# Kernel tuning notes

Hardware: AMD Instinct MI355X
Metric: run time of the kernel (lower is better)

The kernel has to match this reference:

```python
import jax, jax.numpy as jnp
import numpy as np

S, B, L, D, H, NOP = 4, 8, 512, 128, 128, 64  # segments, batch, seg_len, input_dim, hidden, n_operators
W = S * L  # 2048 total words
FT = 0.1   # forget-gate floor


def _norm_mat(m):
    # divide each row by its count of nonzero entries (torch normalize_matrix)
    cnt = (m != 0).sum(-1, keepdims=True).astype(m.dtype)
    return m / (cnt + 1e-30)


def _l2(x):
    return x / (jnp.linalg.norm(x, axis=-1, keepdims=True) + 1e-30)


def setup_inputs() -> dict:
    key = jax.random.key(0)
    ks = jax.random.split(key, 16)
    word_outputs = jax.random.normal(ks[0], (S, B, L, D), jnp.float32)
    node_hidden = jax.random.normal(ks[1], (B, D), jnp.float32)
    op_embedding = jax.random.normal(ks[2], (B, NOP, D), jnp.float32)
    word_operator = (jax.random.uniform(ks[3], (B, W, NOP)) < 0.05).astype(jnp.float32)
    word_word = (jax.random.uniform(ks[4], (B, W, W)) < 0.02).astype(jnp.float32)
    depend_relation = (jax.random.uniform(ks[5], (S, B, L, L)) < 0.05).astype(jnp.float32)
    word_exist_matrix = (jax.random.uniform(ks[6], (B, W, W)) < 0.9).astype(jnp.float32)
    word_exist_sequence = (jax.random.uniform(ks[7], (B, W)) < 0.9).astype(jnp.float32)
    goal_word = (jax.random.uniform(ks[8], (B, W)) < 0.2).astype(jnp.float32)

    def lin(k, fi, fo):
        k1, k2 = jax.random.split(k)
        s = 1.0 / np.sqrt(fi).astype(np.float32)
        return (jax.random.uniform(k1, (fi, fo), jnp.float32, -s, s),
                jax.random.uniform(k2, (fo,), jnp.float32, -s, s))

    o_w_W, o_w_b = lin(ks[9], D, H)
    wk_W, wk_b = lin(ks[10], D, H)
    ws_W, ws_b = lin(ks[11], D, H)
    up_W, up_b = lin(ks[12], 3 * H, D)
    wg_W, wg_b = lin(ks[13], D, D)
    fg_W, fg_b = lin(ks[14], 2 * D, D)
    return dict(word_outputs=word_outputs, node_hidden=node_hidden, op_embedding=op_embedding,
                word_operator=word_operator, word_word=word_word, depend_relation=depend_relation,
                word_exist_matrix=word_exist_matrix, word_exist_sequence=word_exist_sequence,
                goal_word=goal_word, o_w_W=o_w_W, o_w_b=o_w_b, wk_W=wk_W, wk_b=wk_b,
                ws_W=ws_W, ws_b=ws_b, up_W=up_W, up_b=up_b, wg_W=wg_W, wg_b=wg_b,
                fg_W=fg_W, fg_b=fg_b)


def reference(word_outputs, node_hidden, op_embedding, word_operator, word_word,
              depend_relation, word_exist_matrix, word_exist_sequence, goal_word,
              o_w_W, o_w_b, wk_W, wk_b, ws_W, ws_b, up_W, up_b, wg_W, wg_b, fg_W, fg_b):
    # cat(word_outputs, dim=1) -> [B, W, D]
    all_word = word_outputs.transpose(1, 0, 2, 3).reshape(B, W, D)
    # operator aggregation: [B,W,NOP] @ o_w(op_embedding) -> [B,W,H], L2-normalized
    word_o = _l2(jnp.einsum('bwo,boh->bwh', word_operator, op_embedding @ o_w_W + o_w_b))
    # knowledge aggregation over masked word-word adjacency
    adj_k = _norm_mat(word_word * word_exist_matrix)
    word_w_k = _l2(jnp.einsum('bvw,bwh->bvh', adj_k, all_word @ wk_W + wk_b))
    # per-segment dependency aggregation, then concat along word dim
    seg = jnp.einsum('sbij,sbjh->sbih', _norm_mat(depend_relation), word_outputs @ ws_W + ws_b)
    word_w_s = _l2(seg.transpose(1, 0, 2, 3).reshape(B, W, H))
    neighbor = jnp.concatenate([word_o, word_w_k, word_w_s], axis=-1)  # [B, W, 3H]
    word_updated = jax.nn.relu(neighbor @ up_W + up_b)  # [B, W, D]
    # goal pooling: bmm([B,1,W],[B,W,D]) -> [B,D]
    gw = _norm_mat(goal_word * word_exist_sequence)
    goal_w = jnp.einsum('bw,bwd->bd', gw, word_updated)
    goal_updated = jax.nn.relu(goal_w @ wg_W + wg_b)
    forget = jax.nn.sigmoid(jnp.concatenate([goal_w, node_hidden], axis=-1) @ fg_W + fg_b)
    return jnp.maximum(forget, FT) * node_hidden + (1.0 - forget) * goal_updated
```

## Files before the change

### kernel.cpp

```cpp
#include <hip/hip_runtime.h>
#include <math.h>

#define Sn 4
#define Bn 8
#define Ln 512
#define Dn 128
#define Hn 128
#define NOPn 64
#define Wn 2048


__device__ __forceinline__ float bf2f(unsigned short u) {
    return __uint_as_float(((unsigned int)u) << 16);
}
__device__ __forceinline__ float bflo(unsigned int u) {
    return __uint_as_float(u << 16);
}
__device__ __forceinline__ float bfhi(unsigned int u) {
    return __uint_as_float(u & 0xFFFF0000u);
}
__device__ __forceinline__ unsigned short f2bf(float f) {
    unsigned int u = __float_as_uint(f);
    return (unsigned short)((u + 0x7FFFu + ((u >> 16) & 1u)) >> 16);
}

typedef __attribute__((ext_vector_type(8))) short bf16x8;
typedef __attribute__((ext_vector_type(4))) float f32x4;

__global__ __launch_bounds__(256) void prep_k(const float* __restrict__ A,
                                              const float* __restrict__ W1,
                                              const float* __restrict__ W2,
                                              const float* __restrict__ b1,
                                              const float* __restrict__ b2,
                                              unsigned short* __restrict__ C1,
                                              unsigned short* __restrict__ C2,
                                              const float* __restrict__ ope,
                                              const float* __restrict__ owW,
                                              const float* __restrict__ owb,
                                              unsigned short* __restrict__ oph,
                                              const float* __restrict__ goal,
                                              const float* __restrict__ wes,
                                              int* __restrict__ widx,
                                              int* __restrict__ wcnt,
                                              float* __restrict__ gwacc,
                                              const float* __restrict__ upW,
                                              unsigned short* __restrict__ upWbf) {
    __shared__ __align__(16) unsigned char smem[33792];
    const int bid = blockIdx.x, tid = threadIdx.x;

    if (bid < 256) {
        unsigned short (*WT)[132] = reinterpret_cast<unsigned short(*)[132]>(smem);
        const int m0 = bid * 64;
        const int lane = tid & 63, wr = tid >> 6;
        const int rloc = lane & 15, bsel = lane >> 4;

        bf16x8 af[4];
        const float* Arow = A + (size_t)(m0 + wr * 16 + rloc) * 128;
#pragma unroll
        for (int ks = 0; ks < 4; ++ks) {
            float4 a0 = *reinterpret_cast<const float4*>(Arow + ks * 32 + 4 * bsel);
            float4 a1 = *reinterpret_cast<const float4*>(Arow + ks * 32 + 16 + 4 * bsel);
            af[ks][0] = (short)f2bf(a0.x); af[ks][1] = (short)f2bf(a0.y);
            af[ks][2] = (short)f2bf(a0.z); af[ks][3] = (short)f2bf(a0.w);
            af[ks][4] = (short)f2bf(a1.x); af[ks][5] = (short)f2bf(a1.y);
            af[ks][6] = (short)f2bf(a1.z); af[ks][7] = (short)f2bf(a1.w);
        }

#pragma unroll
        for (int mat = 0; mat < 2; ++mat) {
            const float* Wsrc = mat ? W2 : W1;
            const float* bias = mat ? b2 : b1;
            unsigned short* Cdst = mat ? C2 : C1;
            __syncthreads();
            for (int idx = tid; idx < 128 * 128; idx += 256) {
                const int k = idx >> 7, c = idx & 127;
                WT[c][k] = f2bf(Wsrc[k * 128 + c]);
            }
            __syncthreads();

            f32x4 acc[8];
#pragma unroll
            for (int tl = 0; tl < 8; ++tl) acc[tl] = (f32x4){0.f, 0.f, 0.f, 0.f};
#pragma unroll
            for (int ks = 0; ks < 4; ++ks) {
#pragma unroll
                for (int tl = 0; tl < 8; ++tl) {
                    const unsigned short* p = &WT[tl * 16 + rloc][ks * 32 + 4 * bsel];
                    bf16x8 bfv;
#pragma unroll
                    for (int j = 0; j < 4; ++j) {
                        bfv[j]     = (short)p[j];
                        bfv[4 + j] = (short)p[16 + j];
                    }
                    acc[tl] = __builtin_amdgcn_mfma_f32_16x16x32_bf16(
                        af[ks], bfv, acc[tl], 0, 0, 0);
                }
            }
#pragma unroll
            for (int tl = 0; tl < 8; ++tl) {
                const int col = tl * 16 + rloc;
                const float bv = bias[col];
#pragma unroll
                for (int q = 0; q < 4; ++q) {
                    const int row = m0 + wr * 16 + bsel * 4 + q;
                    Cdst[(size_t)row * 128 + col] = f2bf(acc[tl][q] + bv);
                }
            }
        }
    } else if (bid < 264) {
        float (*lA)[68]   = reinterpret_cast<float(*)[68]>(smem);
        float (*lW1)[132] = reinterpret_cast<float(*)[132]>(smem + 8704);
        const int m0 = (bid - 256) * 64;
        float acc[4][8] = {};
        const int r0 = (tid & 15) * 4;
        const int h0 = (tid >> 4) * 8;
        for (int k0 = 0; k0 < 128; k0 += 32) {
            __syncthreads();
            {
                const int r = tid >> 2, kk = (tid & 3) * 8;
                const float* src = ope + (size_t)(m0 + r) * 128 + (k0 + kk);
                float4 v0 = reinterpret_cast<const float4*>(src)[0];
                float4 v1 = reinterpret_cast<const float4*>(src)[1];
                lA[kk + 0][r] = v0.x; lA[kk + 1][r] = v0.y;
                lA[kk + 2][r] = v0.z; lA[kk + 3][r] = v0.w;
                lA[kk + 4][r] = v1.x; lA[kk + 5][r] = v1.y;
                lA[kk + 6][r] = v1.z; lA[kk + 7][r] = v1.w;
            }
            {
                const int kk = tid >> 3, hh = (tid & 7) * 16;
                const float* src = owW + (size_t)(k0 + kk) * 128 + hh;
#pragma unroll
                for (int q = 0; q < 4; ++q) {
                    float4 v = reinterpret_cast<const float4*>(src)[q];
                    lW1[kk][hh + 4 * q + 0] = v.x; lW1[kk][hh + 4 * q + 1] = v.y;
                    lW1[kk][hh + 4 * q + 2] = v.z; lW1[kk][hh + 4 * q + 3] = v.w;
                }
            }
            __syncthreads();
#pragma unroll
            for (int k = 0; k < 32; ++k) {
                float4 a  = *reinterpret_cast<const float4*>(&lA[k][r0]);
                float4 w0 = *reinterpret_cast<const float4*>(&lW1[k][h0]);
                float4 w1 = *reinterpret_cast<const float4*>(&lW1[k][h0 + 4]);
                float av[4] = {a.x, a.y, a.z, a.w};
                float wv[8] = {w0.x, w0.y, w0.z, w0.w, w1.x, w1.y, w1.z, w1.w};
#pragma unroll
                for (int i = 0; i < 4; ++i)
#pragma unroll
                    for (int j = 0; j < 8; ++j) acc[i][j] = fmaf(av[i], wv[j], acc[i][j]);
            }
        }
#pragma unroll
        for (int i = 0; i < 4; ++i) {
            alignas(16) unsigned short us[8];
#pragma unroll
            for (int j = 0; j < 8; ++j) us[j] = f2bf(acc[i][j] + owb[h0 + j]);
            *reinterpret_cast<uint4*>(oph + (size_t)(m0 + r0 + i) * 128 + h0) =
                *reinterpret_cast<const uint4*>(us);
        }
    } else if (bid < 272) {
        int* cnt = reinterpret_cast<int*>(smem);
        const int b = bid - 264;
        if (tid == 0) *cnt = 0;
        __syncthreads();
#pragma unroll
        for (int j = 0; j < 8; ++j) {
            const int w = tid * 8 + j;
            if (goal[b * Wn + w] != 0.f && wes[b * Wn + w] != 0.f) {
                const int p = atomicAdd(cnt, 1);
                if (p < 512) widx[b * 512 + p] = w;
            }
        }
        __syncthreads();
        if (tid == 0) wcnt[b] = *cnt < 512 ? *cnt : 512;
    } else if (bid == 272) {
        for (int idx = tid; idx < 1024; idx += 256) gwacc[idx] = 0.f;
    } else {
        const int base = (bid - 273) * 24576;
        for (int e = base + tid * 4; e < base + 24576; e += 1024) {
            float4 v = *reinterpret_cast<const float4*>(upW + e);
            alignas(8) unsigned short u[4] = {f2bf(v.x), f2bf(v.y), f2bf(v.z), f2bf(v.w)};
            *reinterpret_cast<uint2*>(upWbf + e) = *reinterpret_cast<const uint2*>(u);
        }
    }
}

__global__ __launch_bounds__(256) void mega_agg7(const int* __restrict__ widx,
                                                 const int* __restrict__ wcnt,
                                                 const float* __restrict__ ww,
                                                 const float* __restrict__ wem,
                                                 const float* __restrict__ dep,
                                                 const float* __restrict__ wop,
                                                 const unsigned short* __restrict__ oph,
                                                 const unsigned short* __restrict__ wkh,
                                                 const unsigned short* __restrict__ wsh,
                                                 const unsigned short* __restrict__ upWbf,
                                                 const float* __restrict__ upb,
                                                 float* __restrict__ gwacc) {
    const int bid = blockIdx.x;
    const int b = bid & 7, i = bid >> 3;
    if (i >= wcnt[b]) return;
    const int w_dst = widx[b * 512 + i];
    const int t = threadIdx.x;
    const int lane = t & 63, wv = t >> 6;

    __shared__ int kidx[512];
    __shared__ int sidx[256];
    __shared__ int kn, sn;
    __shared__ float part1[4][128];
    __shared__ float part2[4][128];
    __shared__ float nbL[384];
    __shared__ float gp16[16][128];
    if (t == 0) { kn = 0; sn = 0; }
    __syncthreads();

    const float* wwr = ww  + ((size_t)(b * Wn + w_dst)) * Wn;
    const float* wmr = wem + ((size_t)(b * Wn + w_dst)) * Wn;
#pragma unroll
    for (int q = 0; q < 2; ++q) {
        const int e0 = q * 1024 + t * 4;
        float4 v = *reinterpret_cast<const float4*>(wwr + e0);
        float4 m = *reinterpret_cast<const float4*>(wmr + e0);
        float vv[4] = {v.x, v.y, v.z, v.w};
        float mm[4] = {m.x, m.y, m.z, m.w};
#pragma unroll
        for (int j = 0; j < 4; ++j)
            if (vv[j] != 0.f && mm[j] != 0.f) {
                int p = atomicAdd(&kn, 1);
                if (p < 512) kidx[p] = e0 + j;
            }
    }
    const int sD = w_dst >> 9, lD = w_dst & 511;
    if (t < 128) {
        const float* dr = dep + ((size_t)((sD * Bn + b) * Ln + lD)) * Ln + t * 4;
        float4 v = *reinterpret_cast<const float4*>(dr);
        float vv[4] = {v.x, v.y, v.z, v.w};
#pragma unroll
        for (int j = 0; j < 4; ++j)
            if (vv[j] != 0.f) {
                int p = atomicAdd(&sn, 1);
                if (p < 256) sidx[p] = t * 4 + j;
            }
    }
    float m_op = 0.f;
    if (wv == 3) m_op = wop[((size_t)(b * Wn + w_dst)) * NOPn + lane];
    __syncthreads();

    const int nk = kn < 512 ? kn : 512;
    const int ns = sn < 256 ? sn : 256;

    {
        const int hl = lane >> 5, c = lane & 31;
        float a0 = 0.f, a1 = 0.f, a2 = 0.f, a3 = 0.f;
        for (int p = wv * 2 + hl; p < nk; p += 8) {
            const int w = kidx[p];
            const int s = w >> 9, l = w & 511;
            ushort4 x = *reinterpret_cast<const ushort4*>(
                wkh + ((size_t)((s * Bn + b) * Ln + l)) * Hn + c * 4);
            a0 += bf2f(x.x); a1 += bf2f(x.y); a2 += bf2f(x.z); a3 += bf2f(x.w);
        }
        a0 += __shfl_xor(a0, 32); a1 += __shfl_xor(a1, 32);
        a2 += __shfl_xor(a2, 32); a3 += __shfl_xor(a3, 32);
        if (hl == 0) {
            part1[wv][c * 4 + 0] = a0; part1[wv][c * 4 + 1] = a1;
            part1[wv][c * 4 + 2] = a2; part1[wv][c * 4 + 3] = a3;
        }
    }
    {
        const int hl = lane >> 5, c = lane & 31;
        const unsigned short* base = wsh + (size_t)((sD * Bn + b) * Ln) * Hn + c * 4;
        float a0 = 0.f, a1 = 0.f, a2 = 0.f, a3 = 0.f;
        for (int p = wv * 2 + hl; p < ns; p += 8) {
            ushort4 x = *reinterpret_cast<const ushort4*>(base + (size_t)sidx[p] * Hn);
            a0 += bf2f(x.x); a1 += bf2f(x.y); a2 += bf2f(x.z); a3 += bf2f(x.w);
        }
        a0 += __shfl_xor(a0, 32); a1 += __shfl_xor(a1, 32);
        a2 += __shfl_xor(a2, 32); a3 += __shfl_xor(a3, 32);
        if (hl == 0) {
            part2[wv][c * 4 + 0] = a0; part2[wv][c * 4 + 1] = a1;
            part2[wv][c * 4 + 2] = a2; part2[wv][c * 4 + 3] = a3;
        }
    }
    if (wv == 3) {
        unsigned long long bal = __ballot(m_op != 0.f);
        float a0 = 0.f, a1 = 0.f;
        const unsigned short* base = oph + (size_t)b * NOPn * Hn + 2 * lane;
        while (bal) {
            const int o = __ffsll(bal) - 1;
            bal &= bal - 1;
            ushort2 v = *reinterpret_cast<const ushort2*>(base + o * Hn);
            a0 += bf2f(v.x);
            a1 += bf2f(v.y);
        }
        float ss = a0 * a0 + a1 * a1;
#pragma unroll
        for (int off = 1; off < 64; off <<= 1) ss += __shfl_xor(ss, off);
        const float sc = 1.f / (sqrtf(ss) + 1e-30f);
        nbL[2 * lane]     = a0 * sc;
        nbL[2 * lane + 1] = a1 * sc;
    }
    __syncthreads();

    if (wv == 0) {
        float s0 = 0.f, s1 = 0.f;
#pragma unroll
        for (int q = 0; q < 4; ++q) {
            s0 += part1[q][2 * lane];
            s1 += part1[q][2 * lane + 1];
        }
        float ss = s0 * s0 + s1 * s1;
#pragma unroll
        for (int off = 1; off < 64; off <<= 1) ss += __shfl_xor(ss, off);
        const float sc = 1.f / (sqrtf(ss) + 1e-30f);
        nbL[128 + 2 * lane]     = s0 * sc;
        nbL[128 + 2 * lane + 1] = s1 * sc;
    } else if (wv == 1) {
        float s0 = 0.f, s1 = 0.f;
#pragma unroll
        for (int q = 0; q < 4; ++q) {
            s0 += part2[q][2 * lane];
            s1 += part2[q][2 * lane + 1];
        }
        float ss = s0 * s0 + s1 * s1;
#pragma unroll
        for (int off = 1; off < 64; off <<= 1) ss += __shfl_xor(ss, off);
        const float sc = 1.f / (sqrtf(ss) + 1e-30f);
        nbL[256 + 2 * lane]     = s0 * sc;
        nbL[256 + 2 * lane + 1] = s1 * sc;
    }
    __syncthreads();

    {
        const int i8 = (t & 15) * 8, j = t >> 4;
        float a[8] = {};
#pragma unroll
        for (int r = 0; r < 24; ++r) {
            const int k = r * 16 + j;
            const uint4 w = *reinterpret_cast<const uint4*>(upWbf + (size_t)k * 128 + i8);
            const float x = nbL[k];
            a[0] = fmaf(x, bflo(w.x), a[0]); a[1] = fmaf(x, bfhi(w.x), a[1]);
            a[2] = fmaf(x, bflo(w.y), a[2]); a[3] = fmaf(x, bfhi(w.y), a[3]);
            a[4] = fmaf(x, bflo(w.z), a[4]); a[5] = fmaf(x, bfhi(w.z), a[5]);
            a[6] = fmaf(x, bflo(w.w), a[6]); a[7] = fmaf(x, bfhi(w.w), a[7]);
        }
#pragma unroll
        for (int q = 0; q < 8; ++q) gp16[j][i8 + q] = a[q];
    }
    __syncthreads();
    if (t < 128) {
        float g = upb[t];
#pragma unroll
        for (int j = 0; j < 16; ++j) g += gp16[j][t];
        g = fmaxf(g, 0.f);
        atomicAdd(&gwacc[b * 128 + t], g);
    }
}

__global__ __launch_bounds__(128) void final4_k(const int* __restrict__ wcnt,
                                                const float* __restrict__ gwacc,
                                                const float* __restrict__ nh,
                                                const float* __restrict__ wgW,
                                                const float* __restrict__ wgb,
                                                const float* __restrict__ fgW,
                                                const float* __restrict__ fgb,
                                                float* __restrict__ out) {
    const int b = blockIdx.x, t = threadIdx.x;
    __shared__ float gw[Dn], nhs[Dn];
    const float inv = 1.f / ((float)wcnt[b] + 1e-30f);
    gw[t]  = gwacc[b * Dn + t] * inv;
    nhs[t] = nh[b * Dn + t];
    __syncthreads();
    float gu = wgb[t];
    for (int d = 0; d < Dn; ++d) gu = fmaf(gw[d], wgW[d * Dn + t], gu);
    gu = fmaxf(gu, 0.f);
    float fg = fgb[t];
    for (int d = 0; d < Dn; ++d) fg = fmaf(gw[d], fgW[d * Dn + t], fg);
    for (int d = 0; d < Dn; ++d) fg = fmaf(nhs[d], fgW[(Dn + d) * Dn + t], fg);
    const float forget = 1.f / (1.f + expf(-fg));
    out[b * Dn + t] = fmaxf(forget, 0.1f) * nhs[t] + (1.f - forget) * gu;
}

extern "C" void kernel_launch(void* const* d_in, const int* in_sizes, int n_in,
                              void* d_out, int out_size, void* d_ws, size_t ws_size,
                              hipStream_t stream) {
    (void)in_sizes; (void)n_in; (void)out_size; (void)ws_size;
    const float* word_outputs        = (const float*)d_in[0];
    const float* node_hidden         = (const float*)d_in[1];
    const float* op_embedding        = (const float*)d_in[2];
    const float* word_operator       = (const float*)d_in[3];
    const float* word_word           = (const float*)d_in[4];
    const float* depend_relation     = (const float*)d_in[5];
    const float* word_exist_matrix   = (const float*)d_in[6];
    const float* word_exist_sequence = (const float*)d_in[7];
    const float* goal_word           = (const float*)d_in[8];
    const float* o_w_W = (const float*)d_in[9];
    const float* o_w_b = (const float*)d_in[10];
    const float* wk_W  = (const float*)d_in[11];
    const float* wk_b  = (const float*)d_in[12];
    const float* ws_W  = (const float*)d_in[13];
    const float* ws_b  = (const float*)d_in[14];
    const float* up_W  = (const float*)d_in[15];
    const float* up_b  = (const float*)d_in[16];
    const float* wg_W  = (const float*)d_in[17];
    const float* wg_b  = (const float*)d_in[18];
    const float* fg_W  = (const float*)d_in[19];
    const float* fg_b  = (const float*)d_in[20];
    float* out = (float*)d_out;

    char* ws = (char*)d_ws;
    unsigned short* oph   = (unsigned short*)(ws + 0);
    unsigned short* wkh   = (unsigned short*)(ws + (1u << 20));
    unsigned short* wsh   = (unsigned short*)(ws + (5u << 20));
    int* widx             = (int*)(ws + (9u << 20));
    int* wcnt             = (int*)(ws + (9u << 20) + 32768);
    float* gwacc          = (float*)(ws + (9u << 20) + 65536);
    unsigned short* upWbf = (unsigned short*)(ws + (9u << 20) + 131072);

    prep_k<<<275, 256, 0, stream>>>(word_outputs, wk_W, ws_W, wk_b, ws_b, wkh, wsh,
                                    op_embedding, o_w_W, o_w_b, oph,
                                    goal_word, word_exist_sequence, widx, wcnt, gwacc,
                                    up_W, upWbf);
    mega_agg7<<<4096, 256, 0, stream>>>(widx, wcnt, word_word, word_exist_matrix,
                                        depend_relation, word_operator, oph, wkh, wsh,
                                        upWbf, up_b, gwacc);
    final4_k<<<8, 128, 0, stream>>>(wcnt, gwacc, node_hidden,
                                    wg_W, wg_b, fg_W, fg_b, out);
}
```

Baseline: 334.9 us.

## Replace shared-memory atomic index compaction with per-wave ballot gather; MFMA for op projection

The aggregation kernel no longer builds index lists in shared memory with atomics followed by a block barrier. Each wave scans its own slice of the word-word, mask and dependency rows, ballots the nonzero positions, and gathers the matching hidden rows directly, two rows per iteration split across the half-waves. This removes the atomic contention, the index buffers and one __syncthreads, at the cost of more divergent ballot loops. Separately, the operator-embedding projection blocks in the prep kernel now reuse the bf16 MFMA path instead of a scalar FP32 GEMM, which lowers that projection's precision to bf16 inputs.

Measured after the change: 343.7 us. +2.6%, slower.

```diff
diff --git a/kernel.cpp b/kernel.cpp
--- a/kernel.cpp
+++ b/kernel.cpp
@@ -48,14 +48,16 @@
     __shared__ __align__(16) unsigned char smem[33792];
     const int bid = blockIdx.x, tid = threadIdx.x;
 
-    if (bid < 256) {
+    if (bid < 264) {
         unsigned short (*WT)[132] = reinterpret_cast<unsigned short(*)[132]>(smem);
-        const int m0 = bid * 64;
+        const bool dual = bid < 256;
+        const int m0 = dual ? bid * 64 : (bid - 256) * 64;
+        const float* Asrc = dual ? A : ope;
         const int lane = tid & 63, wr = tid >> 6;
         const int rloc = lane & 15, bsel = lane >> 4;
 
         bf16x8 af[4];
-        const float* Arow = A + (size_t)(m0 + wr * 16 + rloc) * 128;
+        const float* Arow = Asrc + (size_t)(m0 + wr * 16 + rloc) * 128;
 #pragma unroll
         for (int ks = 0; ks < 4; ++ks) {
             float4 a0 = *reinterpret_cast<const float4*>(Arow + ks * 32 + 4 * bsel);
@@ -66,11 +68,11 @@
             af[ks][6] = (short)f2bf(a1.z); af[ks][7] = (short)f2bf(a1.w);
         }
 
-#pragma unroll
-        for (int mat = 0; mat < 2; ++mat) {
-            const float* Wsrc = mat ? W2 : W1;
-            const float* bias = mat ? b2 : b1;
-            unsigned short* Cdst = mat ? C2 : C1;
+        const int nmat = dual ? 2 : 1;
+        for (int mat = 0; mat < nmat; ++mat) {
+            const float* Wsrc = dual ? (mat ? W2 : W1) : owW;
+            const float* bias = dual ? (mat ? b2 : b1) : owb;
+            unsigned short* Cdst = dual ? (mat ? C2 : C1) : oph;
             __syncthreads();
             for (int idx = tid; idx < 128 * 128; idx += 256) {
                 const int k = idx >> 7, c = idx & 127;
@@ -106,57 +108,6 @@
                     Cdst[(size_t)row * 128 + col] = f2bf(acc[tl][q] + bv);
                 }
             }
-        }
-    } else if (bid < 264) {
-        float (*lA)[68]   = reinterpret_cast<float(*)[68]>(smem);
-        float (*lW1)[132] = reinterpret_cast<float(*)[132]>(smem + 8704);
-        const int m0 = (bid - 256) * 64;
-        float acc[4][8] = {};
-        const int r0 = (tid & 15) * 4;
-        const int h0 = (tid >> 4) * 8;
-        for (int k0 = 0; k0 < 128; k0 += 32) {
-            __syncthreads();
-            {
-                const int r = tid >> 2, kk = (tid & 3) * 8;
-                const float* src = ope + (size_t)(m0 + r) * 128 + (k0 + kk);
-                float4 v0 = reinterpret_cast<const float4*>(src)[0];
-                float4 v1 = reinterpret_cast<const float4*>(src)[1];
-                lA[kk + 0][r] = v0.x; lA[kk + 1][r] = v0.y;
-                lA[kk + 2][r] = v0.z; lA[kk + 3][r] = v0.w;
-                lA[kk + 4][r] = v1.x; lA[kk + 5][r] = v1.y;
-                lA[kk + 6][r] = v1.z; lA[kk + 7][r] = v1.w;
-            }
-            {
-                const int kk = tid >> 3, hh = (tid & 7) * 16;
-                const float* src = owW + (size_t)(k0 + kk) * 128 + hh;
-#pragma unroll
-                for (int q = 0; q < 4; ++q) {
-                    float4 v = reinterpret_cast<const float4*>(src)[q];
-                    lW1[kk][hh + 4 * q + 0] = v.x; lW1[kk][hh + 4 * q + 1] = v.y;
-                    lW1[kk][hh + 4 * q + 2] = v.z; lW1[kk][hh + 4 * q + 3] = v.w;
-                }
-            }
-            __syncthreads();
-#pragma unroll
-            for (int k = 0; k < 32; ++k) {
-                float4 a  = *reinterpret_cast<const float4*>(&lA[k][r0]);
-                float4 w0 = *reinterpret_cast<const float4*>(&lW1[k][h0]);
-                float4 w1 = *reinterpret_cast<const float4*>(&lW1[k][h0 + 4]);
-                float av[4] = {a.x, a.y, a.z, a.w};
-                float wv[8] = {w0.x, w0.y, w0.z, w0.w, w1.x, w1.y, w1.z, w1.w};
-#pragma unroll
-                for (int i = 0; i < 4; ++i)
-#pragma unroll
-                    for (int j = 0; j < 8; ++j) acc[i][j] = fmaf(av[i], wv[j], acc[i][j]);
-            }
-        }
-#pragma unroll
-        for (int i = 0; i < 4; ++i) {
-            alignas(16) unsigned short us[8];
-#pragma unroll
-            for (int j = 0; j < 8; ++j) us[j] = f2bf(acc[i][j] + owb[h0 + j]);
-            *reinterpret_cast<uint4*>(oph + (size_t)(m0 + r0 + i) * 128 + h0) =
-                *reinterpret_cast<const uint4*>(us);
         }
     } else if (bid < 272) {
         int* cnt = reinterpret_cast<int*>(smem);
@@ -185,79 +136,64 @@
     }
 }
 
-__global__ __launch_bounds__(256) void mega_agg7(const int* __restrict__ widx,
-                                                 const int* __restrict__ wcnt,
-                                                 const float* __restrict__ ww,
-                                                 const float* __restrict__ wem,
-                                                 const float* __restrict__ dep,
-                                                 const float* __restrict__ wop,
-                                                 const unsigned short* __restrict__ oph,
-                                                 const unsigned short* __restrict__ wkh,
-                                                 const unsigned short* __restrict__ wsh,
-                                                 const unsigned short* __restrict__ upWbf,
-                                                 const float* __restrict__ upb,
-                                                 float* __restrict__ gwacc) {
+__global__ __launch_bounds__(256) void mega_agg10(const int* __restrict__ widx,
+                                                  const int* __restrict__ wcnt,
+                                                  const float* __restrict__ ww,
+                                                  const float* __restrict__ wem,
+                                                  const float* __restrict__ dep,
+                                                  const float* __restrict__ wop,
+                                                  const unsigned short* __restrict__ oph,
+                                                  const unsigned short* __restrict__ wkh,
+                                                  const unsigned short* __restrict__ wsh,
+                                                  const unsigned short* __restrict__ upWbf,
+                                                  const float* __restrict__ upb,
+                                                  float* __restrict__ gwacc) {
     const int bid = blockIdx.x;
     const int b = bid & 7, i = bid >> 3;
     if (i >= wcnt[b]) return;
     const int w_dst = widx[b * 512 + i];
     const int t = threadIdx.x;
     const int lane = t & 63, wv = t >> 6;
-
-    __shared__ int kidx[512];
-    __shared__ int sidx[256];
-    __shared__ int kn, sn;
+    const int hl = lane >> 5, c = lane & 31;
+
     __shared__ float part1[4][128];
     __shared__ float part2[4][128];
     __shared__ float nbL[384];
     __shared__ float gp16[16][128];
-    if (t == 0) { kn = 0; sn = 0; }
-    __syncthreads();
-
-    const float* wwr = ww  + ((size_t)(b * Wn + w_dst)) * Wn;
-    const float* wmr = wem + ((size_t)(b * Wn + w_dst)) * Wn;
-#pragma unroll
-    for (int q = 0; q < 2; ++q) {
-        const int e0 = q * 1024 + t * 4;
-        float4 v = *reinterpret_cast<const float4*>(wwr + e0);
-        float4 m = *reinterpret_cast<const float4*>(wmr + e0);
-        float vv[4] = {v.x, v.y, v.z, v.w};
-        float mm[4] = {m.x, m.y, m.z, m.w};
-#pragma unroll
-        for (int j = 0; j < 4; ++j)
-            if (vv[j] != 0.f && mm[j] != 0.f) {
-                int p = atomicAdd(&kn, 1);
-                if (p < 512) kidx[p] = e0 + j;
-            }
-    }
+
     const int sD = w_dst >> 9, lD = w_dst & 511;
-    if (t < 128) {
-        const float* dr = dep + ((size_t)((sD * Bn + b) * Ln + lD)) * Ln + t * 4;
-        float4 v = *reinterpret_cast<const float4*>(dr);
-        float vv[4] = {v.x, v.y, v.z, v.w};
-#pragma unroll
-        for (int j = 0; j < 4; ++j)
-            if (vv[j] != 0.f) {
-                int p = atomicAdd(&sn, 1);
-                if (p < 256) sidx[p] = t * 4 + j;
-            }
-    }
-    float m_op = 0.f;
-    if (wv == 3) m_op = wop[((size_t)(b * Wn + w_dst)) * NOPn + lane];
-    __syncthreads();
-
-    const int nk = kn < 512 ? kn : 512;
-    const int ns = sn < 256 ? sn : 256;
 
     {
-        const int hl = lane >> 5, c = lane & 31;
+        const float* wwr = ww  + ((size_t)(b * Wn + w_dst)) * Wn;
+        const float* wmr = wem + ((size_t)(b * Wn + w_dst)) * Wn;
         float a0 = 0.f, a1 = 0.f, a2 = 0.f, a3 = 0.f;
-        for (int p = wv * 2 + hl; p < nk; p += 8) {
-            const int w = kidx[p];
-            const int s = w >> 9, l = w & 511;
-            ushort4 x = *reinterpret_cast<const ushort4*>(
-                wkh + ((size_t)((s * Bn + b) * Ln + l)) * Hn + c * 4);
-            a0 += bf2f(x.x); a1 += bf2f(x.y); a2 += bf2f(x.z); a3 += bf2f(x.w);
+#pragma unroll
+        for (int r = 0; r < 2; ++r) {
+            const int e0 = wv * 512 + r * 256 + lane * 4;
+            float4 v = *reinterpret_cast<const float4*>(wwr + e0);
+            float4 m = *reinterpret_cast<const float4*>(wmr + e0);
+            float vv[4] = {v.x, v.y, v.z, v.w};
+            float mm[4] = {m.x, m.y, m.z, m.w};
+#pragma unroll
+            for (int j = 0; j < 4; ++j) {
+                unsigned long long bal = __ballot(vv[j] != 0.f && mm[j] != 0.f);
+                const int base = wv * 512 + r * 256 + j;
+                while (bal) {
+                    const int o0 = __ffsll(bal) - 1;
+                    bal &= bal - 1;
+                    int o1 = -1;
+                    if (bal) { o1 = __ffsll(bal) - 1; bal &= bal - 1; }
+                    const int o = hl ? o1 : o0;
+                    if (o >= 0) {
+                        const int w = base + 4 * o;
+                        const int s = w >> 9, l = w & 511;
+                        ushort4 x = *reinterpret_cast<const ushort4*>(
+                            wkh + ((size_t)((s * Bn + b) * Ln + l)) * Hn + c * 4);
+                        a0 += bf2f(x.x); a1 += bf2f(x.y);
+                        a2 += bf2f(x.z); a3 += bf2f(x.w);
+                    }
+                }
+            }
         }
         a0 += __shfl_xor(a0, 32); a1 += __shfl_xor(a1, 32);
         a2 += __shfl_xor(a2, 32); a3 += __shfl_xor(a3, 32);
@@ -266,13 +202,31 @@
             part1[wv][c * 4 + 2] = a2; part1[wv][c * 4 + 3] = a3;
         }
     }
+
     {
-        const int hl = lane >> 5, c = lane & 31;
-        const unsigned short* base = wsh + (size_t)((sD * Bn + b) * Ln) * Hn + c * 4;
+        const float* dr = dep + ((size_t)((sD * Bn + b) * Ln + lD)) * Ln;
+        const unsigned short* basep = wsh + (size_t)((sD * Bn + b) * Ln) * Hn + c * 4;
         float a0 = 0.f, a1 = 0.f, a2 = 0.f, a3 = 0.f;
-        for (int p = wv * 2 + hl; p < ns; p += 8) {
-            ushort4 x = *reinterpret_cast<const ushort4*>(base + (size_t)sidx[p] * Hn);
-            a0 += bf2f(x.x); a1 += bf2f(x.y); a2 += bf2f(x.z); a3 += bf2f(x.w);
+        const int e0 = wv * 128 + lane * 2;
+        float2 v = *reinterpret_cast<const float2*>(dr + e0);
+        float vv[2] = {v.x, v.y};
+#pragma unroll
+        for (int j = 0; j < 2; ++j) {
+            unsigned long long bal = __ballot(vv[j] != 0.f);
+            const int lbase = wv * 128 + j;
+            while (bal) {
+                const int o0 = __ffsll(bal) - 1;
+                bal &= bal - 1;
+                int o1 = -1;
+                if (bal) { o1 = __ffsll(bal) - 1; bal &= bal - 1; }
+                const int o = hl ? o1 : o0;
+                if (o >= 0) {
+                    const int l = lbase + 2 * o;
+                    ushort4 x = *reinterpret_cast<const ushort4*>(basep + (size_t)l * Hn);
+                    a0 += bf2f(x.x); a1 += bf2f(x.y);
+                    a2 += bf2f(x.z); a3 += bf2f(x.w);
+                }
+            }
         }
         a0 += __shfl_xor(a0, 32); a1 += __shfl_xor(a1, 32);
         a2 += __shfl_xor(a2, 32); a3 += __shfl_xor(a3, 32);
@@ -281,7 +235,9 @@
             part2[wv][c * 4 + 2] = a2; part2[wv][c * 4 + 3] = a3;
         }
     }
+
     if (wv == 3) {
+        const float m_op = wop[((size_t)(b * Wn + w_dst)) * NOPn + lane];
         unsigned long long bal = __ballot(m_op != 0.f);
         float a0 = 0.f, a1 = 0.f;
         const unsigned short* base = oph + (size_t)b * NOPn * Hn + 2 * lane;
@@ -420,9 +376,9 @@
                                     op_embedding, o_w_W, o_w_b, oph,
                                     goal_word, word_exist_sequence, widx, wcnt, gwacc,
                                     up_W, upWbf);
-    mega_agg7<<<4096, 256, 0, stream>>>(widx, wcnt, word_word, word_exist_matrix,
-                                        depend_relation, word_operator, oph, wkh, wsh,
-                                        upWbf, up_b, gwacc);
+    mega_agg10<<<4096, 256, 0, stream>>>(widx, wcnt, word_word, word_exist_matrix,
+                                         depend_relation, word_operator, oph, wkh, wsh,
+                                         upWbf, up_b, gwacc);
     final4_k<<<8, 128, 0, stream>>>(wcnt, gwacc, node_hidden,
                                     wg_W, wg_b, fg_W, fg_b, out);
 }
```
